# Kernel tuning notes

Measured on AMD Instinct MI355X. Metric: run time of the kernel, lower is better.

The kernel has to match this reference:

```python
import jax, jax.numpy as jnp
import numpy as np

B, L, IN_DIM, H, LAYERS = 16, 2048, 64, 512, 4
KERNELS = (5, 11, 23)
EPS_BN, EPS_LN = 1e-5, 1e-5


def setup_inputs() -> dict:
    key = jax.random.key(0)
    ks = jax.random.split(key, 16)
    def n(k, shape, s=0.02):
        return jax.random.normal(k, shape, jnp.float32) * s
    inp = {"x": jax.random.normal(ks[0], (B, L, IN_DIM), jnp.float32)}
    inp["Wp"] = n(ks[1], (H, IN_DIM), 0.1)
    inp["bp"] = jnp.zeros((H,), jnp.float32)
    inp["ln_g"] = jnp.ones((LAYERS, H), jnp.float32)
    inp["ln_b"] = jnp.zeros((LAYERS, H), jnp.float32)
    for i, k in enumerate(KERNELS):
        inp[f"conv_w{i}"] = n(ks[2 + i], (LAYERS, H, k), 0.1)  # depthwise kernels
        inp[f"conv_b{i}"] = jnp.zeros((LAYERS, H), jnp.float32)
    inp["bn_g"] = jnp.ones((LAYERS, 3, H), jnp.float32)
    inp["bn_b"] = jnp.zeros((LAYERS, 3, H), jnp.float32)
    inp["gate_W"] = n(ks[5], (LAYERS, 3, 3 * H), 0.02)
    inp["gate_b"] = jnp.zeros((LAYERS, 3), jnp.float32)
    inp["Wih"] = n(ks[6], (LAYERS, 3 * H, H), 0.04)  # GRU input weights (r,z,n)
    inp["Whh"] = n(ks[7], (LAYERS, 3 * H, H), 0.04)  # GRU hidden weights
    inp["bih"] = jnp.zeros((LAYERS, 3 * H), jnp.float32)
    inp["bhh"] = jnp.zeros((LAYERS, 3 * H), jnp.float32)
    return inp


def _layernorm(h, g, b):
    mu = h.mean(-1, keepdims=True)
    var = ((h - mu) ** 2).mean(-1, keepdims=True)
    return (h - mu) / jnp.sqrt(var + EPS_LN) * g + b


def _dwconv(h_bhl, w, b):
    # h_bhl: [B,H,L]; w: [H,k] depthwise; 'same' padding for odd k (pad=k//2)
    k = w.shape[-1]
    out = jax.lax.conv_general_dilated(
        h_bhl, w[:, None, :], (1,), [(k // 2, k // 2)],
        dimension_numbers=("NCH", "OIH", "NCH"), feature_group_count=h_bhl.shape[1])
    return out + b[None, :, None]


def _longconv_mix(h, conv_ws, conv_bs, bn_g, bn_b, gate_W, gate_b):
    # h: [B,L,H]
    ht = jnp.swapaxes(h, 1, 2)  # [B,H,L]
    bn_scale = 1.0 / jnp.sqrt(1.0 + EPS_BN)  # eval BN: running mean 0, var 1
    outs = []
    for i in range(len(conv_ws)):
        o = _dwconv(ht, conv_ws[i], conv_bs[i])
        o = o * (bn_g[i] * bn_scale)[None, :, None] + bn_b[i][None, :, None]
        outs.append(jax.nn.gelu(o, approximate=False))
    cat_t = jnp.swapaxes(jnp.concatenate(outs, axis=1), 1, 2)  # [B,L,3H]
    logits = cat_t @ gate_W.T + gate_b                          # [B,L,3]
    wgt = jax.nn.softmax(logits, axis=-1)
    stack = jnp.stack(outs, axis=1)                             # [B,3,H,L]
    out = jnp.einsum("bkhl,blk->bhl", stack, wgt)
    return jnp.swapaxes(out, 1, 2)  # [B,L,H]


def _gru(h, Wih, Whh, bih, bhh):
    # torch nn.GRU math, gate order r,z,n; h: [B,L,H]
    Bb, Ll, Hh = h.shape
    xg = jnp.swapaxes(h @ Wih.T + bih, 0, 1)  # [L,B,3H]
    def step(hp, x_t):
        hg = hp @ Whh.T + bhh
        xr, xz, xn = jnp.split(x_t, 3, axis=-1)
        hr, hz, hn = jnp.split(hg, 3, axis=-1)
        r = jax.nn.sigmoid(xr + hr)
        z = jax.nn.sigmoid(xz + hz)
        n = jnp.tanh(xn + r * hn)
        hnew = (1.0 - z) * n + z * hp
        return hnew, hnew
    _, ys = jax.lax.scan(step, jnp.zeros((Bb, Hh), h.dtype), xg)
    return jnp.swapaxes(ys, 0, 1)  # [B,L,H]


def reference(x, Wp, bp, ln_g, ln_b, conv_w0, conv_b0, conv_w1, conv_b1,
              conv_w2, conv_b2, bn_g, bn_b, gate_W, gate_b, Wih, Whh, bih, bhh):
    h = x @ Wp.T + bp  # input_proj: [B,L,H]
    for l in range(LAYERS):
        h = _layernorm(h, ln_g[l], ln_b[l])
        h = _longconv_mix(h,
                          (conv_w0[l], conv_w1[l], conv_w2[l]),
                          (conv_b0[l], conv_b1[l], conv_b2[l]),
                          bn_g[l], bn_b[l], gate_W[l], gate_b[l])
        out = _gru(h, Wih[l], Whh[l], bih[l], bhh[l])
        h = h + out  # residual (dropout=0 in eval)
    return h
```

## Files before the change

kernel.cpp:

```cpp
#include <hip/hip_runtime.h>
#include <hip/hip_bf16.h>


#define B_   16
#define L_   2048
#define IN_  64
#define H_   512
#define H3_  1536
#define NL_  4

typedef unsigned short u16;
typedef unsigned long long u64;
typedef short bf16x8 __attribute__((ext_vector_type(8)));
typedef float f32x4 __attribute__((ext_vector_type(4)));

__device__ __forceinline__ u16 f2bf(float f) {
  unsigned u = __float_as_uint(f);
  u = u + 0x7fffu + ((u >> 16) & 1u);
  return (u16)(u >> 16);
}
__device__ __forceinline__ float bf2f(u16 v) {
  return __uint_as_float(((unsigned)v) << 16);
}
__device__ __forceinline__ float gelu_exact(float x) {
  return 0.5f * x * (1.f + erff(x * 0.70710678118654752440f));
}
__device__ __forceinline__ float sigmoidf_(float x) {
  return 1.f / (1.f + expf(-x));
}

__global__ void k_init(u64* hst, int n) {
  int i = blockIdx.x * blockDim.x + threadIdx.x;
  if (i < n) hst[i] = 0ull;
}

__global__ void k_cvt(const float* __restrict__ in, u16* __restrict__ out, int n) {
  int i = blockIdx.x * blockDim.x + threadIdx.x;
  int stride = gridDim.x * blockDim.x;
  for (; i < n; i += stride) out[i] = f2bf(in[i]);
}

__global__ __launch_bounds__(512)
void k_proj(const float* __restrict__ x, const float* __restrict__ Wp,
            const float* __restrict__ bp, float* __restrict__ hb) {
  __shared__ float4 xs[128];
  const int tid = threadIdx.x;
  const size_t m0 = (size_t)blockIdx.x * 8;
  if (tid < 128) xs[tid] = ((const float4*)(x + m0 * IN_))[tid];
  __syncthreads();
  float4 wv[16];
  const float4* wp4 = (const float4*)(Wp + (size_t)tid * IN_);
#pragma unroll
  for (int i = 0; i < 16; ++i) wv[i] = wp4[i];
  float acc[8] = {0.f,0.f,0.f,0.f,0.f,0.f,0.f,0.f};
#pragma unroll
  for (int k = 0; k < 16; ++k) {
    float4 w4 = wv[k];
#pragma unroll
    for (int rr = 0; rr < 8; ++rr) {
      float4 xv = xs[rr * 16 + k];
      acc[rr] += w4.x * xv.x + w4.y * xv.y + w4.z * xv.z + w4.w * xv.w;
    }
  }
  float bpv = bp[tid];
#pragma unroll
  for (int rr = 0; rr < 8; ++rr) hb[(m0 + rr) * H_ + tid] = acc[rr] + bpv;
}

__global__ __launch_bounds__(256)
void k_ln(const float* __restrict__ hin, const float* __restrict__ g,
          const float* __restrict__ bta, float* __restrict__ lnout) {
  const int w = threadIdx.x >> 6, lane = threadIdx.x & 63;
  const size_t m = (size_t)blockIdx.x * 4 + w;
  const float4* src = (const float4*)(hin + m * H_);
  float4 a = src[lane * 2], c = src[lane * 2 + 1];
  float sm = a.x + a.y + a.z + a.w + c.x + c.y + c.z + c.w;
  float sq = a.x*a.x + a.y*a.y + a.z*a.z + a.w*a.w + c.x*c.x + c.y*c.y + c.z*c.z + c.w*c.w;
  sm += __shfl_xor(sm, 1);  sq += __shfl_xor(sq, 1);
  sm += __shfl_xor(sm, 2);  sq += __shfl_xor(sq, 2);
  sm += __shfl_xor(sm, 4);  sq += __shfl_xor(sq, 4);
  sm += __shfl_xor(sm, 8);  sq += __shfl_xor(sq, 8);
  sm += __shfl_xor(sm, 16); sq += __shfl_xor(sq, 16);
  sm += __shfl_xor(sm, 32); sq += __shfl_xor(sq, 32);
  float mu = sm * (1.f / 512.f);
  float var = sq * (1.f / 512.f) - mu * mu;
  float inv = 1.f / sqrtf(var + 1e-5f);
  const float4* g4 = (const float4*)g;
  const float4* b4 = (const float4*)bta;
  float4 ga = g4[lane * 2], gc = g4[lane * 2 + 1];
  float4 ba = b4[lane * 2], bc = b4[lane * 2 + 1];
  float4 oa, oc;
  oa.x = (a.x - mu) * inv * ga.x + ba.x;
  oa.y = (a.y - mu) * inv * ga.y + ba.y;
  oa.z = (a.z - mu) * inv * ga.z + ba.z;
  oa.w = (a.w - mu) * inv * ga.w + ba.w;
  oc.x = (c.x - mu) * inv * gc.x + bc.x;
  oc.y = (c.y - mu) * inv * gc.y + bc.y;
  oc.z = (c.z - mu) * inv * gc.z + bc.z;
  oc.w = (c.w - mu) * inv * gc.w + bc.w;
  float4* dst = (float4*)(lnout + m * H_);
  dst[lane * 2] = oa;
  dst[lane * 2 + 1] = oc;
}

__global__ __launch_bounds__(512)
void k_mix(const float* __restrict__ ln,
           const float* __restrict__ w0, const float* __restrict__ cb0,
           const float* __restrict__ w1, const float* __restrict__ cb1,
           const float* __restrict__ w2, const float* __restrict__ cb2,
           const float* __restrict__ bng, const float* __restrict__ bnb,
           const float* __restrict__ gW, const float* __restrict__ gb,
           u16* __restrict__ mixbf) {
  const int h = threadIdx.x;
  const int bi = blockIdx.x >> 11;
  const int t = blockIdx.x & (L_ - 1);
  const size_t mrow = (size_t)blockIdx.x;
  float v[23];
#pragma unroll
  for (int d = 0; d < 23; ++d) {
    int tt = t + d - 11;
    v[d] = (tt >= 0 && tt < L_) ? ln[((size_t)bi * L_ + tt) * H_ + h] : 0.f;
  }
  float o0 = cb0[h], o1 = cb1[h], o2 = cb2[h];
#pragma unroll
  for (int d = 0; d < 5; ++d) o0 += v[9 + d] * w0[h * 5 + d];
#pragma unroll
  for (int d = 0; d < 11; ++d) o1 += v[6 + d] * w1[h * 11 + d];
#pragma unroll
  for (int d = 0; d < 23; ++d) o2 += v[d] * w2[h * 23 + d];
  const float bscale = 0.99999500003749968f;
  o0 = o0 * (bng[0 * H_ + h] * bscale) + bnb[0 * H_ + h];
  o1 = o1 * (bng[1 * H_ + h] * bscale) + bnb[1 * H_ + h];
  o2 = o2 * (bng[2 * H_ + h] * bscale) + bnb[2 * H_ + h];
  o0 = gelu_exact(o0); o1 = gelu_exact(o1); o2 = gelu_exact(o2);
  float l0 = o0 * gW[0 * H3_ + h] + o1 * gW[0 * H3_ + H_ + h] + o2 * gW[0 * H3_ + 2 * H_ + h];
  float l1 = o0 * gW[1 * H3_ + h] + o1 * gW[1 * H3_ + H_ + h] + o2 * gW[1 * H3_ + 2 * H_ + h];
  float l2 = o0 * gW[2 * H3_ + h] + o1 * gW[2 * H3_ + H_ + h] + o2 * gW[2 * H3_ + 2 * H_ + h];
  l0 += __shfl_xor(l0, 1);  l1 += __shfl_xor(l1, 1);  l2 += __shfl_xor(l2, 1);
  l0 += __shfl_xor(l0, 2);  l1 += __shfl_xor(l1, 2);  l2 += __shfl_xor(l2, 2);
  l0 += __shfl_xor(l0, 4);  l1 += __shfl_xor(l1, 4);  l2 += __shfl_xor(l2, 4);
  l0 += __shfl_xor(l0, 8);  l1 += __shfl_xor(l1, 8);  l2 += __shfl_xor(l2, 8);
  l0 += __shfl_xor(l0, 16); l1 += __shfl_xor(l1, 16); l2 += __shfl_xor(l2, 16);
  l0 += __shfl_xor(l0, 32); l1 += __shfl_xor(l1, 32); l2 += __shfl_xor(l2, 32);
  __shared__ float red[8][3];
  const int w = h >> 6, lane = h & 63;
  if (lane == 0) { red[w][0] = l0; red[w][1] = l1; red[w][2] = l2; }
  __syncthreads();
  l0 = gb[0]; l1 = gb[1]; l2 = gb[2];
#pragma unroll
  for (int i = 0; i < 8; ++i) { l0 += red[i][0]; l1 += red[i][1]; l2 += red[i][2]; }
  float mx = fmaxf(l0, fmaxf(l1, l2));
  float e0 = expf(l0 - mx), e1 = expf(l1 - mx), e2 = expf(l2 - mx);
  float inv = 1.f / (e0 + e1 + e2);
  float out = (o0 * e0 + o1 * e1 + o2 * e2) * inv;
  mixbf[mrow * H_ + h] = f2bf(out);
}

__global__ __launch_bounds__(256)
void k_gemm(const u16* __restrict__ A, const u16* __restrict__ Bm,
            const float* __restrict__ bias, u16* __restrict__ C) {
  __shared__ u16 As[128 * 32];
  __shared__ u16 Bs[128 * 32];
  const int tid = threadIdx.x;
  const int bm = blockIdx.x / 12, bn = blockIdx.x % 12;
  const int m0 = bm * 128, n0 = bn * 128;
  const int w = tid >> 6, lane = tid & 63;
  const int wr = w >> 1, wc = w & 1;
  const int q = lane >> 4, r = lane & 15;
  f32x4 acc[4][4] = {};
  const uint4* Ag = (const uint4*)(A + (size_t)m0 * H_);
  const uint4* Bg = (const uint4*)(Bm + (size_t)n0 * H_);
  uint4* As4 = (uint4*)As;
  uint4* Bs4 = (uint4*)Bs;
  for (int ko = 0; ko < 16; ++ko) {
    __syncthreads();
#pragma unroll
    for (int i = 0; i < 2; ++i) {
      int j = tid + 256 * i;
      As4[j] = Ag[(size_t)(j >> 2) * 64 + (j & 3) + ko * 4];
      Bs4[j] = Bg[(size_t)(j >> 2) * 64 + (j & 3) + ko * 4];
    }
    __syncthreads();
    bf16x8 av[4], bv[4];
#pragma unroll
    for (int m = 0; m < 4; ++m) av[m] = *(const bf16x8*)&As[(wr * 64 + m * 16 + r) * 32 + q * 8];
#pragma unroll
    for (int n = 0; n < 4; ++n) bv[n] = *(const bf16x8*)&Bs[(wc * 64 + n * 16 + r) * 32 + q * 8];
#pragma unroll
    for (int m = 0; m < 4; ++m)
#pragma unroll
      for (int n = 0; n < 4; ++n)
        acc[m][n] = __builtin_amdgcn_mfma_f32_16x16x32_bf16(av[m], bv[n], acc[m][n], 0, 0, 0);
  }
#pragma unroll
  for (int n = 0; n < 4; ++n) {
    int col = n0 + wc * 64 + n * 16 + r;
    float bv_ = bias[col];
#pragma unroll
    for (int m = 0; m < 4; ++m) {
      int row = m0 + wr * 64 + m * 16 + q * 4;
#pragma unroll
      for (int i = 0; i < 4; ++i) {
        float v = acc[m][n][i] + bv_;
        C[(size_t)(row + i) * H3_ + col] = f2bf(v);
      }
    }
  }
}

__global__ __launch_bounds__(512, 2)
void k_gru(const float* __restrict__ Whh_l, const float* __restrict__ bhh_l,
           const u16* __restrict__ xg, const u16* __restrict__ mixbf,
           float* __restrict__ out_h, u64* hst, int tbase) {
  const int tid = threadIdx.x;
  const int wg = blockIdx.x;
  const int b = wg >> 4;
  const int s = wg & 15;
  const int w = tid >> 6;
  const int lane = tid & 63;
  const int g16 = lane >> 4;
  const int l16 = lane & 15;

  __shared__ float hg_s[96];
  __shared__ __align__(16) float h_s[2][576];

  float wr_[3][32];
  float bh_[3];
#pragma unroll
  for (int q = 0; q < 3; ++q) {
    const int rho = w * 12 + q * 4 + g16;
    const int gate = rho >> 5;
    const int jj = rho & 31;
    const int grow = gate * H_ + s * 32 + jj;
    const float4* wp = (const float4*)(Whh_l + (size_t)grow * H_ + l16 * 32);
#pragma unroll
    for (int c = 0; c < 8; ++c) {
      float4 v = wp[c];
      wr_[q][4 * c + 0] = v.x; wr_[q][4 * c + 1] = v.y;
      wr_[q][4 * c + 2] = v.z; wr_[q][4 * c + 3] = v.w;
    }
    bh_[q] = bhh_l[grow];
  }

  h_s[0][(tid >> 5) * 36 + (tid & 31)] = 0.f;
  float hp = 0.f;
  __syncthreads();

  const int PSTRIDE = B_ * H_;

  for (int t = 0; t < L_; ++t) {
    u16 xr_u = 0, xz_u = 0, xn_u = 0, mx_u = 0;
    size_t orow = ((size_t)b * L_ + t) * H_ + s * 32 + lane;
    if (w == 0 && lane < 32) {
      size_t xb = ((size_t)b * L_ + t) * H3_ + s * 32 + lane;
      xr_u = xg[xb];
      xz_u = xg[xb + H_];
      xn_u = xg[xb + 2 * H_];
      mx_u = mixbf[orow];
    }
    float p0 = 0.f, p1 = 0.f, p2 = 0.f;
    const float* hrow = &h_s[t & 1][l16 * 36];
#pragma unroll
    for (int c = 0; c < 8; ++c) {
      float4 hv = *(const float4*)(hrow + c * 4);
      p0 += wr_[0][4*c]*hv.x + wr_[0][4*c+1]*hv.y + wr_[0][4*c+2]*hv.z + wr_[0][4*c+3]*hv.w;
      p1 += wr_[1][4*c]*hv.x + wr_[1][4*c+1]*hv.y + wr_[1][4*c+2]*hv.z + wr_[1][4*c+3]*hv.w;
      p2 += wr_[2][4*c]*hv.x + wr_[2][4*c+1]*hv.y + wr_[2][4*c+2]*hv.z + wr_[2][4*c+3]*hv.w;
    }
    p0 += __shfl_xor(p0, 1); p1 += __shfl_xor(p1, 1); p2 += __shfl_xor(p2, 1);
    p0 += __shfl_xor(p0, 2); p1 += __shfl_xor(p1, 2); p2 += __shfl_xor(p2, 2);
    p0 += __shfl_xor(p0, 4); p1 += __shfl_xor(p1, 4); p2 += __shfl_xor(p2, 4);
    p0 += __shfl_xor(p0, 8); p1 += __shfl_xor(p1, 8); p2 += __shfl_xor(p2, 8);
    if (l16 == 0) {
      hg_s[w * 12 + 0 + g16] = p0 + bh_[0];
      hg_s[w * 12 + 4 + g16] = p1 + bh_[1];
      hg_s[w * 12 + 8 + g16] = p2 + bh_[2];
    }
    __syncthreads();

    if (w == 0 && lane < 32) {
      const int jj = lane;
      float hr = hg_s[jj], hz = hg_s[32 + jj], hn = hg_s[64 + jj];
      float r = sigmoidf_(bf2f(xr_u) + hr);
      float z = sigmoidf_(bf2f(xz_u) + hz);
      float n = tanhf(bf2f(xn_u) + r * hn);
      float hnew = (1.f - z) * n + z * hp;
      hp = hnew;
      out_h[orow] = bf2f(mx_u) + hnew;
      u64 pv = ((u64)(unsigned)(tbase + t + 1) << 32) | (u64)__float_as_uint(hnew);
      __hip_atomic_store(&hst[(size_t)((t + 1) & 1) * PSTRIDE + (size_t)b * H_ + s * 32 + jj],
                         pv, __ATOMIC_RELAXED, __HIP_MEMORY_SCOPE_AGENT);
    }

    if (t + 1 < L_) {
      const unsigned T = (unsigned)(tbase + t + 1);
      u64* sl = &hst[(size_t)((t + 1) & 1) * PSTRIDE + (size_t)b * H_ + tid];
      u64 v;
      do {
        v = __hip_atomic_load(sl, __ATOMIC_RELAXED, __HIP_MEMORY_SCOPE_AGENT);
      } while ((unsigned)(v >> 32) != T);
      h_s[(t + 1) & 1][(tid >> 5) * 36 + (tid & 31)] = __uint_as_float((unsigned)v);
    }
    __syncthreads();
  }
}

extern "C" void kernel_launch(void* const* d_in, const int* in_sizes, int n_in,
                              void* d_out, int out_size, void* d_ws, size_t ws_size,
                              hipStream_t stream) {
  (void)in_sizes; (void)n_in; (void)out_size; (void)ws_size;
  const float* x    = (const float*)d_in[0];
  const float* Wp   = (const float*)d_in[1];
  const float* bp   = (const float*)d_in[2];
  const float* ln_g = (const float*)d_in[3];
  const float* ln_b = (const float*)d_in[4];
  const float* cw0  = (const float*)d_in[5];
  const float* cb0  = (const float*)d_in[6];
  const float* cw1  = (const float*)d_in[7];
  const float* cb1  = (const float*)d_in[8];
  const float* cw2  = (const float*)d_in[9];
  const float* cb2  = (const float*)d_in[10];
  const float* bng  = (const float*)d_in[11];
  const float* bnb  = (const float*)d_in[12];
  const float* gW   = (const float*)d_in[13];
  const float* gb   = (const float*)d_in[14];
  const float* Wih  = (const float*)d_in[15];
  const float* Whh  = (const float*)d_in[16];
  const float* bih  = (const float*)d_in[17];
  const float* bhh  = (const float*)d_in[18];

  char* ws = (char*)d_ws;
  u16*   xg    = (u16*)(ws + 0);
  float* ln    = (float*)(ws + 0);
  u16*   mixbf = (u16*)(ws + (size_t)96 * 1024 * 1024);
  u16*   wihbf = (u16*)(ws + (size_t)128 * 1024 * 1024);
  u64*   hst   = (u64*)(ws + (size_t)134 * 1024 * 1024);
  float* hbuf  = (float*)d_out;

  k_init<<<dim3(64), dim3(256), 0, stream>>>(hst, 2 * B_ * H_);
  k_cvt<<<dim3(3072), dim3(256), 0, stream>>>(Wih, wihbf, NL_ * H3_ * H_);
  k_proj<<<dim3(B_ * L_ / 8), dim3(512), 0, stream>>>(x, Wp, bp, hbuf);

  for (int l = 0; l < NL_; ++l) {
    k_ln<<<dim3(B_ * L_ / 4), dim3(256), 0, stream>>>(hbuf, ln_g + l * H_, ln_b + l * H_, ln);
    k_mix<<<dim3(B_ * L_), dim3(512), 0, stream>>>(ln,
        cw0 + l * H_ * 5,  cb0 + l * H_,
        cw1 + l * H_ * 11, cb1 + l * H_,
        cw2 + l * H_ * 23, cb2 + l * H_,
        bng + l * 3 * H_, bnb + l * 3 * H_,
        gW + l * 3 * H3_, gb + l * 3, mixbf);
    k_gemm<<<dim3((B_ * L_ / 128) * (H3_ / 128)), dim3(256), 0, stream>>>(
        mixbf, wihbf + (size_t)l * H3_ * H_, bih + l * H3_, xg);

    const float* whh_l = Whh + (size_t)l * H3_ * H_;
    const float* bhh_l = bhh + l * H3_;
    const u16* xg_c = xg;
    const u16* mix_c = mixbf;
    float* outp = hbuf;
    int tbase = l * L_;
    void* args[] = { (void*)&whh_l, (void*)&bhh_l, (void*)&xg_c, (void*)&mix_c,
                     (void*)&outp, (void*)&hst, (void*)&tbase };
    hipLaunchCooperativeKernel((void*)k_gru, dim3(B_ * 16), dim3(512), args, 0, stream);
  }
}
```

Baseline: 17.20 ms.

## Remove intra-step barrier in GRU; compute gates per-wave, publish own slice locally

Reorganises the GRU step so each wave owns 4 hidden units for all three gates. The gate math then runs directly on the shuffle-reduced sums, which removes the shared-memory handoff and one __syncthreads per timestep. Each block writes its own slice of the new hidden state straight into shared memory and only spins on remote slices. It also swaps in fast sigmoid/tanh via __expf and rcp, remaps block indices so a batch's slices are interleaved across blocks, and drops the 2-blocks occupancy hint. The faster activations lower precision slightly, and the block remap changes how the cross-block polling is spread.

```diff
diff --git a/kernel.cpp b/kernel.cpp
--- a/kernel.cpp
+++ b/kernel.cpp
@@ -25,8 +25,14 @@
 __device__ __forceinline__ float gelu_exact(float x) {
   return 0.5f * x * (1.f + erff(x * 0.70710678118654752440f));
 }
-__device__ __forceinline__ float sigmoidf_(float x) {
-  return 1.f / (1.f + expf(-x));
+__device__ __forceinline__ float fast_sig(float x) {
+  float e = __expf(-x);
+  return __builtin_amdgcn_rcpf(1.f + e);
+}
+__device__ __forceinline__ float fast_tanh(float x) {
+  x = fminf(fmaxf(x, -15.f), 15.f);
+  float e = __expf(2.f * x);
+  return (e - 1.f) * __builtin_amdgcn_rcpf(e + 1.f);
 }
 
 __global__ void k_init(u64* hst, int n) {
@@ -208,30 +214,28 @@
   }
 }
 
-__global__ __launch_bounds__(512, 2)
+__global__ __launch_bounds__(512)
 void k_gru(const float* __restrict__ Whh_l, const float* __restrict__ bhh_l,
            const u16* __restrict__ xg, const u16* __restrict__ mixbf,
            float* __restrict__ out_h, u64* hst, int tbase) {
   const int tid = threadIdx.x;
   const int wg = blockIdx.x;
-  const int b = wg >> 4;
-  const int s = wg & 15;
+  const int b = wg & 15;
+  const int s = wg >> 4;
   const int w = tid >> 6;
   const int lane = tid & 63;
   const int g16 = lane >> 4;
   const int l16 = lane & 15;
-
-  __shared__ float hg_s[96];
+  const int jj = 4 * w + g16;
+  const bool gl = (l16 == 0);
+
   __shared__ __align__(16) float h_s[2][576];
 
   float wr_[3][32];
   float bh_[3];
 #pragma unroll
   for (int q = 0; q < 3; ++q) {
-    const int rho = w * 12 + q * 4 + g16;
-    const int gate = rho >> 5;
-    const int jj = rho & 31;
-    const int grow = gate * H_ + s * 32 + jj;
+    const int grow = q * H_ + s * 32 + jj;
     const float4* wp = (const float4*)(Whh_l + (size_t)grow * H_ + l16 * 32);
 #pragma unroll
     for (int c = 0; c < 8; ++c) {
@@ -247,12 +251,13 @@
   __syncthreads();
 
   const int PSTRIDE = B_ * H_;
+  const bool remote = ((tid >> 5) != s);
 
   for (int t = 0; t < L_; ++t) {
     u16 xr_u = 0, xz_u = 0, xn_u = 0, mx_u = 0;
-    size_t orow = ((size_t)b * L_ + t) * H_ + s * 32 + lane;
-    if (w == 0 && lane < 32) {
-      size_t xb = ((size_t)b * L_ + t) * H3_ + s * 32 + lane;
+    size_t orow = ((size_t)b * L_ + t) * H_ + s * 32 + jj;
+    if (gl) {
+      size_t xb = ((size_t)b * L_ + t) * H3_ + s * 32 + jj;
       xr_u = xg[xb];
       xz_u = xg[xb + H_];
       xn_u = xg[xb + 2 * H_];
@@ -271,28 +276,23 @@
     p0 += __shfl_xor(p0, 2); p1 += __shfl_xor(p1, 2); p2 += __shfl_xor(p2, 2);
     p0 += __shfl_xor(p0, 4); p1 += __shfl_xor(p1, 4); p2 += __shfl_xor(p2, 4);
     p0 += __shfl_xor(p0, 8); p1 += __shfl_xor(p1, 8); p2 += __shfl_xor(p2, 8);
-    if (l16 == 0) {
-      hg_s[w * 12 + 0 + g16] = p0 + bh_[0];
-      hg_s[w * 12 + 4 + g16] = p1 + bh_[1];
-      hg_s[w * 12 + 8 + g16] = p2 + bh_[2];
-    }
-    __syncthreads();
-
-    if (w == 0 && lane < 32) {
-      const int jj = lane;
-      float hr = hg_s[jj], hz = hg_s[32 + jj], hn = hg_s[64 + jj];
-      float r = sigmoidf_(bf2f(xr_u) + hr);
-      float z = sigmoidf_(bf2f(xz_u) + hz);
-      float n = tanhf(bf2f(xn_u) + r * hn);
-      float hnew = (1.f - z) * n + z * hp;
+
+    if (gl) {
+      float r = fast_sig(bf2f(xr_u) + p0 + bh_[0]);
+      float z = fast_sig(bf2f(xz_u) + p1 + bh_[1]);
+      float n = fast_tanh(bf2f(xn_u) + r * (p2 + bh_[2]));
+      float hnew = n + z * (hp - n);
       hp = hnew;
       out_h[orow] = bf2f(mx_u) + hnew;
-      u64 pv = ((u64)(unsigned)(tbase + t + 1) << 32) | (u64)__float_as_uint(hnew);
-      __hip_atomic_store(&hst[(size_t)((t + 1) & 1) * PSTRIDE + (size_t)b * H_ + s * 32 + jj],
-                         pv, __ATOMIC_RELAXED, __HIP_MEMORY_SCOPE_AGENT);
-    }
-
-    if (t + 1 < L_) {
+      h_s[(t + 1) & 1][s * 36 + jj] = hnew;
+      if (t + 1 < L_) {
+        u64 pv = ((u64)(unsigned)(tbase + t + 1) << 32) | (u64)__float_as_uint(hnew);
+        __hip_atomic_store(&hst[(size_t)((t + 1) & 1) * PSTRIDE + (size_t)b * H_ + s * 32 + jj],
+                           pv, __ATOMIC_RELAXED, __HIP_MEMORY_SCOPE_AGENT);
+      }
+    }
+
+    if (remote && t + 1 < L_) {
       const unsigned T = (unsigned)(tbase + t + 1);
       u64* sl = &hst[(size_t)((t + 1) & 1) * PSTRIDE + (size_t)b * H_ + tid];
       u64 v;
```

After: 30.09 ms. +74.9%, slower.
